# Performance work log

Measured on AMD Instinct MI355X. Metric: run time of the kernel, lower is better.

The kernel has to match this reference:

```python
import jax, jax.numpy as jnp
import numpy as np

N_NODES = 50000
N_EDGES = 800000
N_GRAPHS = 500
DIM = 64          # node feature dim
NG = 64           # num gaussians (edge rbf dim)
CUTOFF = 12.0
NCONV = 3
HID = 128
NTYPES = 100      # atom vocabulary for embedding
EPS = 1e-5        # batchnorm eps


def _bn(x, g, b):
    # training-mode batchnorm over the leading (edge/node) axis
    m = jnp.mean(x, axis=0)
    v = jnp.var(x, axis=0)
    return g * (x - m) * jax.lax.rsqrt(v + EPS) + b


def setup_inputs() -> dict:
    key = jax.random.key(0)
    ks = jax.random.split(key, 12)
    atom_types = jax.random.randint(ks[0], (N_NODES,), 0, NTYPES)
    src = jax.random.randint(ks[1], (N_EDGES,), 0, N_NODES)
    dst = jax.random.randint(ks[2], (N_EDGES,), 0, N_NODES)
    graph_ids = jnp.sort(jax.random.randint(ks[3], (N_NODES,), 0, N_GRAPHS))
    distance = jax.random.uniform(ks[4], (N_EDGES,), dtype=jnp.float32) * CUTOFF
    cin = 2 * DIM + NG
    s = 0.05
    embed_table = jax.random.normal(ks[5], (NTYPES, DIM), dtype=jnp.float32) * s
    W1 = jax.random.normal(ks[6], (NCONV, cin, DIM), dtype=jnp.float32) * s
    b1 = jnp.zeros((NCONV, DIM), jnp.float32)
    W2 = jax.random.normal(ks[7], (NCONV, cin, DIM), dtype=jnp.float32) * s
    b2 = jnp.zeros((NCONV, DIM), jnp.float32)
    g1 = jnp.ones((NCONV, DIM), jnp.float32); bt1 = jnp.zeros((NCONV, DIM), jnp.float32)
    g2 = jnp.ones((NCONV, DIM), jnp.float32); bt2 = jnp.zeros((NCONV, DIM), jnp.float32)
    g3 = jnp.ones((NCONV, DIM), jnp.float32); bt3 = jnp.zeros((NCONV, DIM), jnp.float32)
    Wfc = jax.random.normal(ks[8], (DIM, HID), dtype=jnp.float32) * s
    bfc = jnp.zeros((HID,), jnp.float32)
    Wout = jax.random.normal(ks[9], (HID, 1), dtype=jnp.float32) * s
    bout = jnp.zeros((1,), jnp.float32)
    return dict(atom_types=atom_types, src=src, dst=dst, graph_ids=graph_ids,
                distance=distance, embed_table=embed_table,
                W1=W1, b1=b1, W2=W2, b2=b2,
                g1=g1, bt1=bt1, g2=g2, bt2=bt2, g3=g3, bt3=bt3,
                Wfc=Wfc, bfc=bfc, Wout=Wout, bout=bout)


def reference(atom_types, src, dst, graph_ids, distance, embed_table,
              W1, b1, W2, b2, g1, bt1, g2, bt2, g3, bt3,
              Wfc, bfc, Wout, bout):
    # embedding lookup
    node = embed_table[atom_types]                           # [N, DIM]
    # RBF expansion of distances (gaussian smearing on [0, CUTOFF])
    mu = jnp.linspace(0.0, CUTOFF, NG, dtype=jnp.float32)
    coeff = -0.5 / (mu[1] - mu[0]) ** 2
    rbf = jnp.exp(coeff * (distance[:, None] - mu) ** 2)      # [E, NG]

    for i in range(NCONV):
        # gather: concat(src feats, dst feats, edge rbf)
        te = jnp.concatenate([node[src], node[dst], rbf], axis=-1)  # [E, 192]
        nbr_filter = jax.nn.sigmoid(_bn(te @ W1[i] + b1[i], g1[i], bt1[i]))
        # NOTE: faithful to the source bug: bn2 is applied to nbr_filter,
        # so fc_full2 (W2/b2) output is computed in torch but unused.
        nbr_core = jax.nn.softplus(_bn(nbr_filter, g2[i], bt2[i]))
        h = nbr_filter * nbr_core                              # [E, DIM]
        # scatter-sum messages to destination nodes
        agg = jax.ops.segment_sum(h, dst, num_segments=N_NODES)
        node = node + _bn(agg, g3[i], bt3[i])

    # avg pooling per graph
    sums = jax.ops.segment_sum(node, graph_ids, num_segments=N_GRAPHS)
    cnts = jax.ops.segment_sum(jnp.ones((N_NODES, 1), node.dtype), graph_ids,
                               num_segments=N_GRAPHS)
    crys = sums / jnp.maximum(cnts, 1.0)                       # [G, DIM]

    crys = jax.nn.softplus(crys) @ Wfc + bfc
    crys = jax.nn.softplus(crys)
    return crys @ Wout + bout                                  # [G, 1]
```

## Files before the change

### kernel.cpp

```cpp
#include <hip/hip_runtime.h>
#include <hip/hip_fp16.h>
#include <math.h>

#define DIM 64
#define NG 64
#define CIN 192
#define HID 128
#define NCONV 3
#define TB 2048
#define CUTOFF 12.0f
#define EPS 1e-5f
#define SCB 256

typedef int i2v __attribute__((ext_vector_type(2)));
typedef int i4v __attribute__((ext_vector_type(4)));

__device__ __forceinline__ float sp_(float y) {
    return fmaxf(y, 0.f) + __logf(1.f + __expf(-fabsf(y)));
}
__device__ __forceinline__ float sig_(float y) {
    return 1.f / (1.f + __expf(-y));
}
__device__ __forceinline__ float2 h2f2_bits(int bits) {
    __half2 h;
    __builtin_memcpy(&h, &bits, 4);
    return __half22float2(h);
}
__device__ __forceinline__ int f2h2_bits(float a, float b) {
    __half2 h;
    h.x = __float2half(a);
    h.y = __float2half(b);
    int r;
    __builtin_memcpy(&r, &h, 4);
    return r;
}

__global__ void k_tables(const float* __restrict__ W1, __half2* __restrict__ Tp) {
    int row = blockIdx.x;
    int l = row / TB, i = row % TB;
    int d = threadIdx.x;
    const float stepmu = CUTOFF / (float)(NG - 1);
    const float coeff = -0.5f / (stepmu * stepmu);
    const float stepx = CUTOFF / (float)(TB - 1);
    float x0 = (float)i * stepx;
    float x1 = fminf((float)(i + 1), (float)(TB - 1)) * stepx;
    __shared__ float r0[NG];
    __shared__ float r1[NG];
    float mu = (float)d * stepmu;
    float d0 = x0 - mu, d1 = x1 - mu;
    r0[d] = expf(coeff * d0 * d0);
    r1[d] = expf(coeff * d1 * d1);
    __syncthreads();
    const float* w = W1 + (size_t)(l * CIN + 2 * DIM) * DIM;
    float a0 = 0.f, a1 = 0.f;
#pragma unroll 8
    for (int g = 0; g < NG; ++g) {
        float wv = w[g * DIM + d];
        a0 += r0[g] * wv;
        a1 += r1[g] * wv;
    }
    __half2 hh;
    hh.x = __float2half(a0);
    hh.y = __float2half(a1);
    Tp[(size_t)row * DIM + d] = hh;
}

__global__ void k_hist(const int* __restrict__ dst, int* __restrict__ cnt, int E) {
    for (int e = blockIdx.x * blockDim.x + threadIdx.x; e < E;
         e += gridDim.x * blockDim.x)
        atomicAdd(&cnt[dst[e]], 1);
}

__global__ void k_scanA(const int* __restrict__ cnt, int* __restrict__ bsum, int N) {
    __shared__ int lds[SCB];
    int i = blockIdx.x * SCB + threadIdx.x;
    lds[threadIdx.x] = (i < N) ? cnt[i] : 0;
    __syncthreads();
    for (int o = SCB / 2; o > 0; o >>= 1) {
        if (threadIdx.x < o) lds[threadIdx.x] += lds[threadIdx.x + o];
        __syncthreads();
    }
    if (threadIdx.x == 0) bsum[blockIdx.x] = lds[0];
}

__global__ void k_scanB(const int* __restrict__ bsum, int* __restrict__ bexcl, int NB) {
    __shared__ int lds[SCB];
    int t = threadIdx.x;
    int v = (t < NB) ? bsum[t] : 0;
    lds[t] = v;
    __syncthreads();
    for (int o = 1; o < SCB; o <<= 1) {
        int add = (t >= o) ? lds[t - o] : 0;
        __syncthreads();
        lds[t] += add;
        __syncthreads();
    }
    if (t < NB) bexcl[t] = lds[t] - v;
}

__global__ void k_scanC(const int* __restrict__ cnt, const int* __restrict__ bexcl,
                        int* __restrict__ off, int* __restrict__ cursor, int N, int E) {
    __shared__ int lds[SCB];
    int t = threadIdx.x;
    int i = blockIdx.x * SCB + t;
    int v = (i < N) ? cnt[i] : 0;
    lds[t] = v;
    __syncthreads();
    for (int o = 1; o < SCB; o <<= 1) {
        int add = (t >= o) ? lds[t - o] : 0;
        __syncthreads();
        lds[t] += add;
        __syncthreads();
    }
    if (i < N) {
        int excl = bexcl[blockIdx.x] + lds[t] - v;
        off[i] = excl;
        cursor[i] = excl;
        if (i == N - 1) off[N] = E;
    }
}

__global__ void k_scatter(const int* __restrict__ src, const int* __restrict__ dst,
                          const float* __restrict__ dist, int* __restrict__ cursor,
                          int2* __restrict__ es, int E) {
    const float inv_step = (float)(TB - 1) / CUTOFF;
    for (int e = blockIdx.x * blockDim.x + threadIdx.x; e < E;
         e += gridDim.x * blockDim.x) {
        int t = dst[e];
        int pos = atomicAdd(&cursor[t], 1);
        es[pos] = make_int2(src[e], __float_as_int(dist[e] * inv_step));
    }
}

template <int FIRST>
__global__ void __launch_bounds__(256) k_pq(
        const int* __restrict__ at, const float* __restrict__ emb,
        float* __restrict__ node, const float* __restrict__ agg,
        const double* __restrict__ st, const float* __restrict__ g3,
        const float* __restrict__ bt3, double invN,
        const float* __restrict__ W1, const float* __restrict__ b1, int l,
        __half* __restrict__ P16, float* __restrict__ Q, int N) {
    __shared__ float wa[DIM * DIM];
    __shared__ float wb[DIM * DIM];
    const float* WA = W1 + (size_t)(l * CIN) * DIM;
    for (int k = threadIdx.x; k < DIM * DIM; k += blockDim.x) {
        wa[k] = WA[k];
        wb[k] = WA[DIM * DIM + k];
    }
    int lane = threadIdx.x & 63, w = threadIdx.x >> 6;
    float bv = b1[lane];
    float a3 = 0.f, c3 = 0.f;
    if (!FIRST) {
        double m = st[lane] * invN;
        double v = st[64 + lane] * invN - m * m;
        a3 = g3[lane] / sqrtf((float)v + EPS);
        c3 = bt3[lane] - a3 * (float)m;
    }
    __syncthreads();
    int wpb = blockDim.x >> 6;
    for (int n = blockIdx.x * wpb + w; n < N; n += gridDim.x * wpb) {
        float nv;
        if (FIRST) {
            nv = emb[at[n] * DIM + lane];
        } else {
            nv = node[n * DIM + lane] + a3 * agg[n * DIM + lane] + c3;
        }
        node[n * DIM + lane] = nv;
        float ap = 0.f, aq = bv;
#pragma unroll 8
        for (int k = 0; k < DIM; ++k) {
            float b = __shfl(nv, k);
            ap += b * wa[k * DIM + lane];
            aq += b * wb[k * DIM + lane];
        }
        P16[n * DIM + lane] = __float2half(ap);
        Q[n * DIM + lane] = aq;
    }
}

__global__ void __launch_bounds__(256) k_convA(
        const int* __restrict__ off, const int2* __restrict__ es,
        const __half* __restrict__ P16, const float* __restrict__ Q,
        const __half2* __restrict__ Tp,
        double* __restrict__ stats, __half* __restrict__ z16, int N) {
    int lane = threadIdx.x & 63;
    int w = threadIdx.x >> 6;
    int dg = lane & 15;
    int slot = lane >> 4;
    int d0 = dg * 4;
    float s00 = 0.f, s01 = 0.f, s02 = 0.f, s03 = 0.f;
    float s10 = 0.f, s11 = 0.f, s12 = 0.f, s13 = 0.f;
    int gw = blockIdx.x * 4 + w, nw = gridDim.x * 4;
    for (int n = gw; n < N; n += nw) {
        int e0 = off[n], e1 = off[n + 1];
        if (e0 >= e1) continue;
        float4 q4 = *(const float4*)(Q + (size_t)n * DIM + d0);
        for (int eb = e0; eb < e1; eb += 8) {
            int eA = eb + slot, eB = eA + 4;
            bool vA = (eA < e1), vB = (eB < e1);
            int2 evA = es[vA ? eA : e1 - 1];
            int2 evB = es[vB ? eB : e1 - 1];
            float uA = __int_as_float(evA.y), uB = __int_as_float(evB.y);
            int iA = (int)uA, iB = (int)uB;
            iA = max(0, min(iA, TB - 2));
            iB = max(0, min(iB, TB - 2));
            float frA = uA - (float)iA, frB = uB - (float)iB;
            i2v pbA = *(const i2v*)(P16 + (size_t)evA.x * DIM + d0);
            i2v pbB = *(const i2v*)(P16 + (size_t)evB.x * DIM + d0);
            i4v tbA = *(const i4v*)(Tp + (size_t)iA * DIM + d0);
            i4v tbB = *(const i4v*)(Tp + (size_t)iB * DIM + d0);
            {
                float2 p01 = h2f2_bits(pbA.x), p23 = h2f2_bits(pbA.y);
                float2 t0 = h2f2_bits(tbA.x), t1 = h2f2_bits(tbA.y);
                float2 t2 = h2f2_bits(tbA.z), t3 = h2f2_bits(tbA.w);
                float z0 = p01.x + t0.x + frA * (t0.y - t0.x) + q4.x;
                float z1 = p01.y + t1.x + frA * (t1.y - t1.x) + q4.y;
                float z2 = p23.x + t2.x + frA * (t2.y - t2.x) + q4.z;
                float z3 = p23.y + t3.x + frA * (t3.y - t3.x) + q4.w;
                if (vA) {
                    i2v zz;
                    zz.x = f2h2_bits(z0, z1);
                    zz.y = f2h2_bits(z2, z3);
                    *(i2v*)(z16 + (size_t)eA * DIM + d0) = zz;
                    s00 += z0; s10 += z0 * z0;
                    s01 += z1; s11 += z1 * z1;
                    s02 += z2; s12 += z2 * z2;
                    s03 += z3; s13 += z3 * z3;
                }
            }
            {
                float2 p01 = h2f2_bits(pbB.x), p23 = h2f2_bits(pbB.y);
                float2 t0 = h2f2_bits(tbB.x), t1 = h2f2_bits(tbB.y);
                float2 t2 = h2f2_bits(tbB.z), t3 = h2f2_bits(tbB.w);
                float z0 = p01.x + t0.x + frB * (t0.y - t0.x) + q4.x;
                float z1 = p01.y + t1.x + frB * (t1.y - t1.x) + q4.y;
                float z2 = p23.x + t2.x + frB * (t2.y - t2.x) + q4.z;
                float z3 = p23.y + t3.x + frB * (t3.y - t3.x) + q4.w;
                if (vB) {
                    i2v zz;
                    zz.x = f2h2_bits(z0, z1);
                    zz.y = f2h2_bits(z2, z3);
                    *(i2v*)(z16 + (size_t)eB * DIM + d0) = zz;
                    s00 += z0; s10 += z0 * z0;
                    s01 += z1; s11 += z1 * z1;
                    s02 += z2; s12 += z2 * z2;
                    s03 += z3; s13 += z3 * z3;
                }
            }
        }
    }
    __shared__ float r0[4][64][4];
    __shared__ float r1[4][64][4];
    r0[w][lane][0] = s00; r0[w][lane][1] = s01;
    r0[w][lane][2] = s02; r0[w][lane][3] = s03;
    r1[w][lane][0] = s10; r1[w][lane][1] = s11;
    r1[w][lane][2] = s12; r1[w][lane][3] = s13;
    __syncthreads();
    if (threadIdx.x < 64) {
        int d = threadIdx.x;
        int dgg = d >> 2, q = d & 3;
        float t0 = 0.f, t1 = 0.f;
#pragma unroll
        for (int ww = 0; ww < 4; ++ww)
#pragma unroll
            for (int sl = 0; sl < 4; ++sl) {
                t0 += r0[ww][sl * 16 + dgg][q];
                t1 += r1[ww][sl * 16 + dgg][q];
            }
        atomicAdd(&stats[d], (double)t0);
        atomicAdd(&stats[64 + d], (double)t1);
    }
}

__global__ void __launch_bounds__(256) k_statsF(
        __half* __restrict__ zf16,
        const double* __restrict__ stA, const float* __restrict__ gA,
        const float* __restrict__ btA,
        double* __restrict__ stats, int total8, double invE) {
    int gq = threadIdx.x & 7;
    float a1[8], c1[8];
#pragma unroll
    for (int q = 0; q < 8; ++q) {
        int d = gq * 8 + q;
        double m = stA[d] * invE;
        double v = stA[64 + d] * invE - m * m;
        a1[q] = gA[d] / sqrtf((float)v + EPS);
        c1[q] = btA[d] - a1[q] * (float)m;
    }
    float s0[8] = {0, 0, 0, 0, 0, 0, 0, 0};
    float s1[8] = {0, 0, 0, 0, 0, 0, 0, 0};
    i4v* z4 = (i4v*)zf16;
    int tid = blockIdx.x * blockDim.x + threadIdx.x;
    int stride = gridDim.x * blockDim.x;
    for (int i = tid; i < total8; i += stride) {
        i4v v = z4[i];
        float2 p0 = h2f2_bits(v.x);
        float2 p1 = h2f2_bits(v.y);
        float2 p2 = h2f2_bits(v.z);
        float2 p3 = h2f2_bits(v.w);
        float f0 = sig_(a1[0] * p0.x + c1[0]);
        float f1 = sig_(a1[1] * p0.y + c1[1]);
        float f2 = sig_(a1[2] * p1.x + c1[2]);
        float f3 = sig_(a1[3] * p1.y + c1[3]);
        float f4 = sig_(a1[4] * p2.x + c1[4]);
        float f5 = sig_(a1[5] * p2.y + c1[5]);
        float f6 = sig_(a1[6] * p3.x + c1[6]);
        float f7 = sig_(a1[7] * p3.y + c1[7]);
        i4v o;
        o.x = f2h2_bits(f0, f1);
        o.y = f2h2_bits(f2, f3);
        o.z = f2h2_bits(f4, f5);
        o.w = f2h2_bits(f6, f7);
        z4[i] = o;
        s0[0] += f0; s1[0] += f0 * f0;
        s0[1] += f1; s1[1] += f1 * f1;
        s0[2] += f2; s1[2] += f2 * f2;
        s0[3] += f3; s1[3] += f3 * f3;
        s0[4] += f4; s1[4] += f4 * f4;
        s0[5] += f5; s1[5] += f5 * f5;
        s0[6] += f6; s1[6] += f6 * f6;
        s0[7] += f7; s1[7] += f7 * f7;
    }
    __shared__ float lds[256][16];
#pragma unroll
    for (int q = 0; q < 8; ++q) {
        lds[threadIdx.x][q] = s0[q];
        lds[threadIdx.x][8 + q] = s1[q];
    }
    __syncthreads();
    if (threadIdx.x < 64) {
        int d = threadIdx.x;
        int grp = d >> 3, j = d & 7;
        float t0 = 0.f, t1 = 0.f;
        for (int k = 0; k < 32; ++k) {
            int t = k * 8 + grp;
            t0 += lds[t][j];
            t1 += lds[t][8 + j];
        }
        atomicAdd(&stats[d], (double)t0);
        atomicAdd(&stats[64 + d], (double)t1);
    }
}

__global__ void __launch_bounds__(256) k_aggF(
        const int* __restrict__ off, const __half* __restrict__ f16,
        const double* __restrict__ stB, const float* __restrict__ gB,
        const float* __restrict__ btB,
        double* __restrict__ stats, float* __restrict__ agg, int N, double invE) {
    int lane = threadIdx.x & 63;
    int w = threadIdx.x >> 6;
    int dg = lane & 7;
    int slot = lane >> 3;
    int d0 = dg * 8;
    float a2[8], c2[8];
#pragma unroll
    for (int q = 0; q < 8; ++q) {
        int d = d0 + q;
        double m = stB[d] * invE, v = stB[64 + d] * invE - m * m;
        a2[q] = gB[d] / sqrtf((float)v + EPS);
        c2[q] = btB[d] - a2[q] * (float)m;
    }
    float s0[8] = {0, 0, 0, 0, 0, 0, 0, 0};
    float s1[8] = {0, 0, 0, 0, 0, 0, 0, 0};
    int gw = blockIdx.x * 4 + w, nw = gridDim.x * 4;
    for (int n = gw; n < N; n += nw) {
        int e0 = off[n], e1 = off[n + 1];
        float tot[8] = {0, 0, 0, 0, 0, 0, 0, 0};
        for (int eb = e0; eb < e1; eb += 16) {
            int eA = eb + slot, eB = eA + 8;
            float mkA = (eA < e1) ? 1.f : 0.f;
            float mkB = (eB < e1) ? 1.f : 0.f;
            int ecA = (eA < e1) ? eA : (e1 - 1);
            int ecB = (eB < e1) ? eB : (e1 - 1);
            i4v zbA = *(const i4v*)(f16 + (size_t)ecA * DIM + d0);
            i4v zbB = *(const i4v*)(f16 + (size_t)ecB * DIM + d0);
            float2 a0 = h2f2_bits(zbA.x), a1v = h2f2_bits(zbA.y);
            float2 a2v = h2f2_bits(zbA.z), a3v = h2f2_bits(zbA.w);
            float2 b0 = h2f2_bits(zbB.x), b1v = h2f2_bits(zbB.y);
            float2 b2v = h2f2_bits(zbB.z), b3v = h2f2_bits(zbB.w);
            float fA[8] = {a0.x, a0.y, a1v.x, a1v.y, a2v.x, a2v.y, a3v.x, a3v.y};
            float fB[8] = {b0.x, b0.y, b1v.x, b1v.y, b2v.x, b2v.y, b3v.x, b3v.y};
#pragma unroll
            for (int q = 0; q < 8; ++q) {
                float hA = fA[q] * sp_(a2[q] * fA[q] + c2[q]);
                float hB = fB[q] * sp_(a2[q] * fB[q] + c2[q]);
                tot[q] += mkA * hA + mkB * hB;
            }
        }
#pragma unroll
        for (int q = 0; q < 8; ++q) {
            float v = tot[q];
            v += __shfl_xor(v, 8);
            v += __shfl_xor(v, 16);
            v += __shfl_xor(v, 32);
            tot[q] = v;
        }
        if (slot == 0) {
            float4 w0 = make_float4(tot[0], tot[1], tot[2], tot[3]);
            float4 w1 = make_float4(tot[4], tot[5], tot[6], tot[7]);
            *(float4*)(agg + (size_t)n * DIM + d0) = w0;
            *(float4*)(agg + (size_t)n * DIM + d0 + 4) = w1;
#pragma unroll
            for (int q = 0; q < 8; ++q) {
                s0[q] += tot[q];
                s1[q] += tot[q] * tot[q];
            }
        }
    }
    __shared__ float r0[4][8][8];
    __shared__ float r1[4][8][8];
    if (slot == 0) {
#pragma unroll
        for (int q = 0; q < 8; ++q) {
            r0[w][dg][q] = s0[q];
            r1[w][dg][q] = s1[q];
        }
    }
    __syncthreads();
    if (threadIdx.x < 64) {
        int d = threadIdx.x;
        int dgg = d >> 3, q = d & 7;
        float t0 = 0.f, t1 = 0.f;
#pragma unroll
        for (int ww = 0; ww < 4; ++ww) {
            t0 += r0[ww][dgg][q];
            t1 += r1[ww][dgg][q];
        }
        atomicAdd(&stats[d], (double)t0);
        atomicAdd(&stats[64 + d], (double)t1);
    }
}

template <int MODE>
__global__ void __launch_bounds__(256) k_conv(
        const int* __restrict__ off, const int2* __restrict__ es,
        const __half* __restrict__ P16, const float* __restrict__ Q,
        const __half2* __restrict__ Tp,
        const double* __restrict__ stA, const float* __restrict__ gA,
        const float* __restrict__ btA,
        const double* __restrict__ stB, const float* __restrict__ gB,
        const float* __restrict__ btB,
        double* __restrict__ stats, float* __restrict__ agg, int N, double invE) {
    int lane = threadIdx.x & 63;
    int w = threadIdx.x >> 6;
    float a1 = 0.f, c1 = 0.f, a2 = 0.f, c2 = 0.f;
    if (MODE >= 2) {
        double m = stA[lane] * invE;
        double v = stA[64 + lane] * invE - m * m;
        a1 = gA[lane] / sqrtf((float)v + EPS);
        c1 = btA[lane] - a1 * (float)m;
    }
    if (MODE == 3) {
        double m = stB[lane] * invE;
        double v = stB[64 + lane] * invE - m * m;
        a2 = gB[lane] / sqrtf((float)v + EPS);
        c2 = btB[lane] - a2 * (float)m;
    }
    float s0 = 0.f, s1 = 0.f;
    int gw = blockIdx.x * 4 + w, nw = gridDim.x * 4;
    for (int n = gw; n < N; n += nw) {
        int e0 = off[n], e1 = off[n + 1];
        float qc = Q[n * DIM + lane];
        float acc = 0.f;
        auto body = [&](int2 ev) {
            float u = __int_as_float(ev.y);
            int i = (int)u;
            i = max(0, min(i, TB - 2));
            float fr = u - (float)i;
            float2 t2 = __half22float2(Tp[(size_t)i * DIM + lane]);
            float p = __half2float(P16[(size_t)ev.x * DIM + lane]);
            float z = p + t2.x + fr * (t2.y - t2.x) + qc;
            if (MODE == 0) { s0 += z; s1 += z * z; }
            else {
                float f = sig_(a1 * z + c1);
                if (MODE == 2) { s0 += f; s1 += f * f; }
                else acc += f * sp_(a2 * f + c2);
            }
        };
        int e = e0;
        for (; e + 2 <= e1; e += 2) { body(es[e]); body(es[e + 1]); }
        if (e < e1) body(es[e]);
        if (MODE == 3) {
            agg[n * DIM + lane] = acc;
            s0 += acc; s1 += acc * acc;
        }
    }
    __shared__ float r0[4][64];
    __shared__ float r1[4][64];
    r0[w][lane] = s0;
    r1[w][lane] = s1;
    __syncthreads();
    if (threadIdx.x < 64) {
        int d = threadIdx.x;
        float t0 = r0[0][d] + r0[1][d] + r0[2][d] + r0[3][d];
        float t1 = r1[0][d] + r1[1][d] + r1[2][d] + r1[3][d];
        atomicAdd(&stats[d], (double)t0);
        atomicAdd(&stats[64 + d], (double)t1);
    }
}

__global__ void k_head(const float* __restrict__ node, const float* __restrict__ agg,
                       const double* __restrict__ st, const float* __restrict__ g3,
                       const float* __restrict__ bt3, double invN,
                       const int* __restrict__ gid, int N,
                       const float* __restrict__ Wfc, const float* __restrict__ bfc,
                       const float* __restrict__ Wout, const float* __restrict__ bout,
                       float* __restrict__ out) {
    int g = blockIdx.x;
    __shared__ int bounds[2];
    if (threadIdx.x == 0) {
        int lo = 0, hi = N;
        while (lo < hi) { int mid = (lo + hi) >> 1; if (gid[mid] < g) lo = mid + 1; else hi = mid; }
        bounds[0] = lo;
        int lo2 = lo; hi = N;
        while (lo2 < hi) { int mid = (lo2 + hi) >> 1; if (gid[mid] < g + 1) lo2 = mid + 1; else hi = mid; }
        bounds[1] = lo2;
    }
    __syncthreads();
    int s = bounds[0], e = bounds[1];
    __shared__ float sp[DIM];
    if (threadIdx.x < DIM) {
        int d = threadIdx.x;
        double mm = st[d] * invN;
        double vv = st[64 + d] * invN - mm * mm;
        float a3 = g3[d] / sqrtf((float)vv + EPS);
        float c3 = bt3[d] - a3 * (float)mm;
        float sn = 0.f, sa = 0.f;
        for (int n = s; n < e; ++n) {
            sn += node[(size_t)n * DIM + d];
            sa += agg[(size_t)n * DIM + d];
        }
        float cntf = (float)max(e - s, 1);
        float m = (sn + a3 * sa) / cntf + c3;
        sp[d] = (m > 0.f) ? m + log1pf(expf(-m)) : log1pf(expf(m));
    }
    __syncthreads();
    int j = threadIdx.x;
    float hj = bfc[j];
#pragma unroll 8
    for (int k = 0; k < DIM; ++k) hj += sp[k] * Wfc[k * HID + j];
    hj = (hj > 0.f) ? hj + log1pf(expf(-hj)) : log1pf(expf(hj));
    __shared__ float red[HID];
    red[j] = hj * Wout[j];
    __syncthreads();
    for (int o = HID / 2; o > 0; o >>= 1) {
        if (j < o) red[j] += red[j + o];
        __syncthreads();
    }
    if (j == 0) out[g] = red[0] + bout[0];
}

extern "C" void kernel_launch(void* const* d_in, const int* in_sizes, int n_in,
                              void* d_out, int out_size, void* d_ws, size_t ws_size,
                              hipStream_t stream) {
    const int* atom_types = (const int*)d_in[0];
    const int* src = (const int*)d_in[1];
    const int* dst = (const int*)d_in[2];
    const int* gid = (const int*)d_in[3];
    const float* dist = (const float*)d_in[4];
    const float* emb = (const float*)d_in[5];
    const float* W1 = (const float*)d_in[6];
    const float* b1 = (const float*)d_in[7];
    const float* g1 = (const float*)d_in[10];
    const float* bt1 = (const float*)d_in[11];
    const float* g2 = (const float*)d_in[12];
    const float* bt2 = (const float*)d_in[13];
    const float* g3 = (const float*)d_in[14];
    const float* bt3 = (const float*)d_in[15];
    const float* Wfc = (const float*)d_in[16];
    const float* bfc = (const float*)d_in[17];
    const float* Wout = (const float*)d_in[18];
    const float* bout = (const float*)d_in[19];

    int N = in_sizes[0];
    int E = in_sizes[1];
    int G = out_size;
    int NB = (N + SCB - 1) / SCB;

    char* ws = (char*)d_ws;
    auto alloc = [&](size_t bytes) -> char* {
        char* p = ws;
        ws += (bytes + 255) & ~(size_t)255;
        return p;
    };
    size_t nd = (size_t)N * DIM * sizeof(float);
    float* node = (float*)alloc(nd);
    __half* P16 = (__half*)alloc(nd / 2);
    float* Q = (float*)alloc(nd);
    float* agg = (float*)alloc(nd);
    __half2* Tp = (__half2*)alloc((size_t)NCONV * TB * DIM * sizeof(__half2));
    double* stats = (double*)alloc((size_t)NCONV * 3 * 128 * sizeof(double));
    int* off = (int*)alloc((size_t)(N + 1) * sizeof(int));
    int* cursor = (int*)alloc((size_t)N * sizeof(int));
    int* cnt = (int*)alloc((size_t)N * sizeof(int));
    int* bsum = (int*)alloc(SCB * sizeof(int));
    int* bexcl = (int*)alloc(SCB * sizeof(int));
    int2* es = (int2*)alloc((size_t)E * sizeof(int2));
    size_t zbytes = (size_t)E * DIM * sizeof(__half);
    size_t used = (size_t)(ws - (char*)d_ws);
    bool planZ = (used + zbytes) <= ws_size;
    __half* z16 = planZ ? (__half*)alloc(zbytes) : nullptr;

    hipMemsetAsync(stats, 0, (size_t)NCONV * 3 * 128 * sizeof(double), stream);
    hipMemsetAsync(cnt, 0, (size_t)N * sizeof(int), stream);

    k_tables<<<NCONV * TB, 64, 0, stream>>>(W1, Tp);

    k_hist<<<1024, 256, 0, stream>>>(dst, cnt, E);
    k_scanA<<<NB, SCB, 0, stream>>>(cnt, bsum, N);
    k_scanB<<<1, SCB, 0, stream>>>(bsum, bexcl, NB);
    k_scanC<<<NB, SCB, 0, stream>>>(cnt, bexcl, off, cursor, N, E);
    k_scatter<<<1024, 256, 0, stream>>>(src, dst, dist, cursor, es, E);

    double invE = 1.0 / (double)E;
    double invN = 1.0 / (double)N;

    for (int l = 0; l < NCONV; ++l) {
        const __half2* Tl = Tp + (size_t)l * TB * DIM;
        double* st1 = stats + (size_t)(l * 3 + 0) * 128;
        double* st2 = stats + (size_t)(l * 3 + 1) * 128;
        double* st3 = stats + (size_t)(l * 3 + 2) * 128;

        if (l == 0) {
            k_pq<1><<<2048, 256, 0, stream>>>(atom_types, emb, node, nullptr,
                                              nullptr, nullptr, nullptr, 0.0,
                                              W1, b1 + l * DIM, l, P16, Q, N);
        } else {
            double* st3p = stats + (size_t)((l - 1) * 3 + 2) * 128;
            k_pq<0><<<2048, 256, 0, stream>>>(atom_types, emb, node, agg,
                                              st3p, g3 + (l - 1) * DIM,
                                              bt3 + (l - 1) * DIM, invN,
                                              W1, b1 + l * DIM, l, P16, Q, N);
        }

        if (planZ) {
            k_convA<<<2048, 256, 0, stream>>>(off, es, P16, Q, Tl, st1, z16, N);
            k_statsF<<<2048, 256, 0, stream>>>(z16, st1, g1 + l * DIM, bt1 + l * DIM,
                                               st2, E * 8, invE);
            k_aggF<<<2048, 256, 0, stream>>>(off, z16,
                                             st2, g2 + l * DIM, bt2 + l * DIM,
                                             st3, agg, N, invE);
        } else {
            k_conv<0><<<2048, 256, 0, stream>>>(off, es, P16, Q, Tl,
                                                nullptr, nullptr, nullptr,
                                                nullptr, nullptr, nullptr,
                                                st1, nullptr, N, invE);
            k_conv<2><<<2048, 256, 0, stream>>>(off, es, P16, Q, Tl,
                                                st1, g1 + l * DIM, bt1 + l * DIM,
                                                nullptr, nullptr, nullptr,
                                                st2, nullptr, N, invE);
            k_conv<3><<<2048, 256, 0, stream>>>(off, es, P16, Q, Tl,
                                                st1, g1 + l * DIM, bt1 + l * DIM,
                                                st2, g2 + l * DIM, bt2 + l * DIM,
                                                st3, agg, N, invE);
        }
    }

    double* st3f = stats + (size_t)(2 * 3 + 2) * 128;
    k_head<<<G, HID, 0, stream>>>(node, agg, st3f, g3 + 2 * DIM, bt3 + 2 * DIM,
                                  invN, gid, N, Wfc, bfc, Wout, bout, (float*)d_out);
}
```

Measured before the change: 971.8 us.

## Flatten edge conv pass over edges and merge scan into one kernel

The first conv pass now loops over the CSR-sorted edges in flat chunks of 8 instead of one wavefront per destination node. It reads each edge's destination from a new dst_s array written during the scatter step, which removes load imbalance from uneven node degrees and the tail waste on low-degree nodes. The cost is an extra per-edge index read plus one Q gather per edge instead of one per node. The three-kernel scan is also replaced by a single 1024-thread block scan, which cuts two launches but runs serially per thread over about 49 elements.

```diff
diff --git a/kernel.cpp b/kernel.cpp
--- a/kernel.cpp
+++ b/kernel.cpp
@@ -10,7 +10,6 @@
 #define TB 2048
 #define CUTOFF 12.0f
 #define EPS 1e-5f
-#define SCB 256
 
 typedef int i2v __attribute__((ext_vector_type(2)));
 typedef int i4v __attribute__((ext_vector_type(4)));
@@ -71,64 +70,43 @@
         atomicAdd(&cnt[dst[e]], 1);
 }
 
-__global__ void k_scanA(const int* __restrict__ cnt, int* __restrict__ bsum, int N) {
-    __shared__ int lds[SCB];
-    int i = blockIdx.x * SCB + threadIdx.x;
-    lds[threadIdx.x] = (i < N) ? cnt[i] : 0;
-    __syncthreads();
-    for (int o = SCB / 2; o > 0; o >>= 1) {
-        if (threadIdx.x < o) lds[threadIdx.x] += lds[threadIdx.x + o];
+__global__ void __launch_bounds__(1024) k_scan(const int* __restrict__ cnt,
+                                               int* __restrict__ off,
+                                               int* __restrict__ cursor,
+                                               int N, int E) {
+    __shared__ int psum[1024];
+    int t = threadIdx.x;
+    int C = (N + 1023) / 1024;
+    int lo = t * C, hi = min(lo + C, N);
+    int s = 0;
+    for (int i = lo; i < hi; ++i) s += cnt[i];
+    psum[t] = s;
+    __syncthreads();
+    for (int o = 1; o < 1024; o <<= 1) {
+        int add = (t >= o) ? psum[t - o] : 0;
         __syncthreads();
-    }
-    if (threadIdx.x == 0) bsum[blockIdx.x] = lds[0];
-}
-
-__global__ void k_scanB(const int* __restrict__ bsum, int* __restrict__ bexcl, int NB) {
-    __shared__ int lds[SCB];
-    int t = threadIdx.x;
-    int v = (t < NB) ? bsum[t] : 0;
-    lds[t] = v;
-    __syncthreads();
-    for (int o = 1; o < SCB; o <<= 1) {
-        int add = (t >= o) ? lds[t - o] : 0;
+        psum[t] += add;
         __syncthreads();
-        lds[t] += add;
-        __syncthreads();
-    }
-    if (t < NB) bexcl[t] = lds[t] - v;
-}
-
-__global__ void k_scanC(const int* __restrict__ cnt, const int* __restrict__ bexcl,
-                        int* __restrict__ off, int* __restrict__ cursor, int N, int E) {
-    __shared__ int lds[SCB];
-    int t = threadIdx.x;
-    int i = blockIdx.x * SCB + t;
-    int v = (i < N) ? cnt[i] : 0;
-    lds[t] = v;
-    __syncthreads();
-    for (int o = 1; o < SCB; o <<= 1) {
-        int add = (t >= o) ? lds[t - o] : 0;
-        __syncthreads();
-        lds[t] += add;
-        __syncthreads();
-    }
-    if (i < N) {
-        int excl = bexcl[blockIdx.x] + lds[t] - v;
-        off[i] = excl;
-        cursor[i] = excl;
-        if (i == N - 1) off[N] = E;
-    }
+    }
+    int run = psum[t] - s;
+    for (int i = lo; i < hi; ++i) {
+        off[i] = run;
+        cursor[i] = run;
+        run += cnt[i];
+    }
+    if (t == 1023) off[N] = E;
 }
 
 __global__ void k_scatter(const int* __restrict__ src, const int* __restrict__ dst,
                           const float* __restrict__ dist, int* __restrict__ cursor,
-                          int2* __restrict__ es, int E) {
+                          int2* __restrict__ es, int* __restrict__ dst_s, int E) {
     const float inv_step = (float)(TB - 1) / CUTOFF;
     for (int e = blockIdx.x * blockDim.x + threadIdx.x; e < E;
          e += gridDim.x * blockDim.x) {
         int t = dst[e];
         int pos = atomicAdd(&cursor[t], 1);
         es[pos] = make_int2(src[e], __float_as_int(dist[e] * inv_step));
+        dst_s[pos] = t;
     }
 }
 
@@ -160,11 +138,8 @@
     int wpb = blockDim.x >> 6;
     for (int n = blockIdx.x * wpb + w; n < N; n += gridDim.x * wpb) {
         float nv;
-        if (FIRST) {
-            nv = emb[at[n] * DIM + lane];
-        } else {
-            nv = node[n * DIM + lane] + a3 * agg[n * DIM + lane] + c3;
-        }
+        if (FIRST) nv = emb[at[n] * DIM + lane];
+        else nv = node[n * DIM + lane] + a3 * agg[n * DIM + lane] + c3;
         node[n * DIM + lane] = nv;
         float ap = 0.f, aq = bv;
 #pragma unroll 8
@@ -178,74 +153,73 @@
     }
 }
 
-__global__ void __launch_bounds__(256) k_convA(
-        const int* __restrict__ off, const int2* __restrict__ es,
+__global__ void __launch_bounds__(256) k_convAf(
+        const int2* __restrict__ es, const int* __restrict__ dst_s,
         const __half* __restrict__ P16, const float* __restrict__ Q,
         const __half2* __restrict__ Tp,
-        double* __restrict__ stats, __half* __restrict__ z16, int N) {
+        double* __restrict__ stats, __half* __restrict__ z16, int E) {
     int lane = threadIdx.x & 63;
     int w = threadIdx.x >> 6;
-    int dg = lane & 15;
-    int slot = lane >> 4;
+    int dg = lane & 15, slot = lane >> 4;
     int d0 = dg * 4;
     float s00 = 0.f, s01 = 0.f, s02 = 0.f, s03 = 0.f;
     float s10 = 0.f, s11 = 0.f, s12 = 0.f, s13 = 0.f;
     int gw = blockIdx.x * 4 + w, nw = gridDim.x * 4;
-    for (int n = gw; n < N; n += nw) {
-        int e0 = off[n], e1 = off[n + 1];
-        if (e0 >= e1) continue;
-        float4 q4 = *(const float4*)(Q + (size_t)n * DIM + d0);
-        for (int eb = e0; eb < e1; eb += 8) {
-            int eA = eb + slot, eB = eA + 4;
-            bool vA = (eA < e1), vB = (eB < e1);
-            int2 evA = es[vA ? eA : e1 - 1];
-            int2 evB = es[vB ? eB : e1 - 1];
-            float uA = __int_as_float(evA.y), uB = __int_as_float(evB.y);
-            int iA = (int)uA, iB = (int)uB;
-            iA = max(0, min(iA, TB - 2));
-            iB = max(0, min(iB, TB - 2));
-            float frA = uA - (float)iA, frB = uB - (float)iB;
-            i2v pbA = *(const i2v*)(P16 + (size_t)evA.x * DIM + d0);
-            i2v pbB = *(const i2v*)(P16 + (size_t)evB.x * DIM + d0);
-            i4v tbA = *(const i4v*)(Tp + (size_t)iA * DIM + d0);
-            i4v tbB = *(const i4v*)(Tp + (size_t)iB * DIM + d0);
-            {
-                float2 p01 = h2f2_bits(pbA.x), p23 = h2f2_bits(pbA.y);
-                float2 t0 = h2f2_bits(tbA.x), t1 = h2f2_bits(tbA.y);
-                float2 t2 = h2f2_bits(tbA.z), t3 = h2f2_bits(tbA.w);
-                float z0 = p01.x + t0.x + frA * (t0.y - t0.x) + q4.x;
-                float z1 = p01.y + t1.x + frA * (t1.y - t1.x) + q4.y;
-                float z2 = p23.x + t2.x + frA * (t2.y - t2.x) + q4.z;
-                float z3 = p23.y + t3.x + frA * (t3.y - t3.x) + q4.w;
-                if (vA) {
-                    i2v zz;
-                    zz.x = f2h2_bits(z0, z1);
-                    zz.y = f2h2_bits(z2, z3);
-                    *(i2v*)(z16 + (size_t)eA * DIM + d0) = zz;
-                    s00 += z0; s10 += z0 * z0;
-                    s01 += z1; s11 += z1 * z1;
-                    s02 += z2; s12 += z2 * z2;
-                    s03 += z3; s13 += z3 * z3;
-                }
+    for (int eb = gw * 8; eb < E; eb += nw * 8) {
+        int eA = eb + slot, eB = eA + 4;
+        bool vA = (eA < E), vB = (eB < E);
+        int ecA = vA ? eA : E - 1;
+        int ecB = vB ? eB : E - 1;
+        int2 evA = es[ecA];
+        int2 evB = es[ecB];
+        int dA = dst_s[ecA], dB = dst_s[ecB];
+        float uA = __int_as_float(evA.y), uB = __int_as_float(evB.y);
+        int iA = (int)uA, iB = (int)uB;
+        iA = max(0, min(iA, TB - 2));
+        iB = max(0, min(iB, TB - 2));
+        float frA = uA - (float)iA, frB = uB - (float)iB;
+        i2v pbA = *(const i2v*)(P16 + (size_t)evA.x * DIM + d0);
+        i2v pbB = *(const i2v*)(P16 + (size_t)evB.x * DIM + d0);
+        i4v tbA = *(const i4v*)(Tp + (size_t)iA * DIM + d0);
+        i4v tbB = *(const i4v*)(Tp + (size_t)iB * DIM + d0);
+        float4 qA = *(const float4*)(Q + (size_t)dA * DIM + d0);
+        float4 qB = *(const float4*)(Q + (size_t)dB * DIM + d0);
+        {
+            float2 p01 = h2f2_bits(pbA.x), p23 = h2f2_bits(pbA.y);
+            float2 t0 = h2f2_bits(tbA.x), t1 = h2f2_bits(tbA.y);
+            float2 t2 = h2f2_bits(tbA.z), t3 = h2f2_bits(tbA.w);
+            float z0 = p01.x + t0.x + frA * (t0.y - t0.x) + qA.x;
+            float z1 = p01.y + t1.x + frA * (t1.y - t1.x) + qA.y;
+            float z2 = p23.x + t2.x + frA * (t2.y - t2.x) + qA.z;
+            float z3 = p23.y + t3.x + frA * (t3.y - t3.x) + qA.w;
+            if (vA) {
+                i2v zz;
+                zz.x = f2h2_bits(z0, z1);
+                zz.y = f2h2_bits(z2, z3);
+                *(i2v*)(z16 + (size_t)eA * DIM + d0) = zz;
+                s00 += z0; s10 += z0 * z0;
+                s01 += z1; s11 += z1 * z1;
+                s02 += z2; s12 += z2 * z2;
+                s03 += z3; s13 += z3 * z3;
             }
-            {
-                float2 p01 = h2f2_bits(pbB.x), p23 = h2f2_bits(pbB.y);
-                float2 t0 = h2f2_bits(tbB.x), t1 = h2f2_bits(tbB.y);
-                float2 t2 = h2f2_bits(tbB.z), t3 = h2f2_bits(tbB.w);
-                float z0 = p01.x + t0.x + frB * (t0.y - t0.x) + q4.x;
-                float z1 = p01.y + t1.x + frB * (t1.y - t1.x) + q4.y;
-                float z2 = p23.x + t2.x + frB * (t2.y - t2.x) + q4.z;
-                float z3 = p23.y + t3.x + frB * (t3.y - t3.x) + q4.w;
-                if (vB) {
-                    i2v zz;
-                    zz.x = f2h2_bits(z0, z1);
-                    zz.y = f2h2_bits(z2, z3);
-                    *(i2v*)(z16 + (size_t)eB * DIM + d0) = zz;
-                    s00 += z0; s10 += z0 * z0;
-                    s01 += z1; s11 += z1 * z1;
-                    s02 += z2; s12 += z2 * z2;
-                    s03 += z3; s13 += z3 * z3;
-                }
+        }
+        {
+            float2 p01 = h2f2_bits(pbB.x), p23 = h2f2_bits(pbB.y);
+            float2 t0 = h2f2_bits(tbB.x), t1 = h2f2_bits(tbB.y);
+            float2 t2 = h2f2_bits(tbB.z), t3 = h2f2_bits(tbB.w);
+            float z0 = p01.x + t0.x + frB * (t0.y - t0.x) + qB.x;
+            float z1 = p01.y + t1.x + frB * (t1.y - t1.x) + qB.y;
+            float z2 = p23.x + t2.x + frB * (t2.y - t2.x) + qB.z;
+            float z3 = p23.y + t3.x + frB * (t3.y - t3.x) + qB.w;
+            if (vB) {
+                i2v zz;
+                zz.x = f2h2_bits(z0, z1);
+                zz.y = f2h2_bits(z2, z3);
+                *(i2v*)(z16 + (size_t)eB * DIM + d0) = zz;
+                s00 += z0; s10 += z0 * z0;
+                s01 += z1; s11 += z1 * z1;
+                s02 += z2; s12 += z2 * z2;
+                s03 += z3; s13 += z3 * z3;
             }
         }
     }
@@ -349,8 +323,7 @@
         double* __restrict__ stats, float* __restrict__ agg, int N, double invE) {
     int lane = threadIdx.x & 63;
     int w = threadIdx.x >> 6;
-    int dg = lane & 7;
-    int slot = lane >> 3;
+    int dg = lane & 7, slot = lane >> 3;
     int d0 = dg * 8;
     float a2[8], c2[8];
 #pragma unroll
@@ -429,6 +402,57 @@
         atomicAdd(&stats[d], (double)t0);
         atomicAdd(&stats[64 + d], (double)t1);
     }
+}
+
+__global__ void k_head(const float* __restrict__ node, const float* __restrict__ agg,
+                       const double* __restrict__ st, const float* __restrict__ g3,
+                       const float* __restrict__ bt3, double invN,
+                       const int* __restrict__ gid, int N,
+                       const float* __restrict__ Wfc, const float* __restrict__ bfc,
+                       const float* __restrict__ Wout, const float* __restrict__ bout,
+                       float* __restrict__ out) {
+    int g = blockIdx.x;
+    __shared__ int bounds[2];
+    if (threadIdx.x == 0) {
+        int lo = 0, hi = N;
+        while (lo < hi) { int mid = (lo + hi) >> 1; if (gid[mid] < g) lo = mid + 1; else hi = mid; }
+        bounds[0] = lo;
+        int lo2 = lo; hi = N;
+        while (lo2 < hi) { int mid = (lo2 + hi) >> 1; if (gid[mid] < g + 1) lo2 = mid + 1; else hi = mid; }
+        bounds[1] = lo2;
+    }
+    __syncthreads();
+    int s = bounds[0], e = bounds[1];
+    __shared__ float sp[DIM];
+    if (threadIdx.x < DIM) {
+        int d = threadIdx.x;
+        double mm = st[d] * invN;
+        double vv = st[64 + d] * invN - mm * mm;
+        float a3 = g3[d] / sqrtf((float)vv + EPS);
+        float c3 = bt3[d] - a3 * (float)mm;
+        float sn = 0.f, sa = 0.f;
+        for (int n = s; n < e; ++n) {
+            sn += node[(size_t)n * DIM + d];
+            sa += agg[(size_t)n * DIM + d];
+        }
+        float cntf = (float)max(e - s, 1);
+        float m = (sn + a3 * sa) / cntf + c3;
+        sp[d] = (m > 0.f) ? m + log1pf(expf(-m)) : log1pf(expf(m));
+    }
+    __syncthreads();
+    int j = threadIdx.x;
+    float hj = bfc[j];
+#pragma unroll 8
+    for (int k = 0; k < DIM; ++k) hj += sp[k] * Wfc[k * HID + j];
+    hj = (hj > 0.f) ? hj + log1pf(expf(-hj)) : log1pf(expf(hj));
+    __shared__ float red[HID];
+    red[j] = hj * Wout[j];
+    __syncthreads();
+    for (int o = HID / 2; o > 0; o >>= 1) {
+        if (j < o) red[j] += red[j + o];
+        __syncthreads();
+    }
+    if (j == 0) out[g] = red[0] + bout[0];
 }
 
 template <int MODE>
@@ -499,57 +523,6 @@
     }
 }
 
-__global__ void k_head(const float* __restrict__ node, const float* __restrict__ agg,
-                       const double* __restrict__ st, const float* __restrict__ g3,
-                       const float* __restrict__ bt3, double invN,
-                       const int* __restrict__ gid, int N,
-                       const float* __restrict__ Wfc, const float* __restrict__ bfc,
-                       const float* __restrict__ Wout, const float* __restrict__ bout,
-                       float* __restrict__ out) {
-    int g = blockIdx.x;
-    __shared__ int bounds[2];
-    if (threadIdx.x == 0) {
-        int lo = 0, hi = N;
-        while (lo < hi) { int mid = (lo + hi) >> 1; if (gid[mid] < g) lo = mid + 1; else hi = mid; }
-        bounds[0] = lo;
-        int lo2 = lo; hi = N;
-        while (lo2 < hi) { int mid = (lo2 + hi) >> 1; if (gid[mid] < g + 1) lo2 = mid + 1; else hi = mid; }
-        bounds[1] = lo2;
-    }
-    __syncthreads();
-    int s = bounds[0], e = bounds[1];
-    __shared__ float sp[DIM];
-    if (threadIdx.x < DIM) {
-        int d = threadIdx.x;
-        double mm = st[d] * invN;
-        double vv = st[64 + d] * invN - mm * mm;
-        float a3 = g3[d] / sqrtf((float)vv + EPS);
-        float c3 = bt3[d] - a3 * (float)mm;
-        float sn = 0.f, sa = 0.f;
-        for (int n = s; n < e; ++n) {
-            sn += node[(size_t)n * DIM + d];
-            sa += agg[(size_t)n * DIM + d];
-        }
-        float cntf = (float)max(e - s, 1);
-        float m = (sn + a3 * sa) / cntf + c3;
-        sp[d] = (m > 0.f) ? m + log1pf(expf(-m)) : log1pf(expf(m));
-    }
-    __syncthreads();
-    int j = threadIdx.x;
-    float hj = bfc[j];
-#pragma unroll 8
-    for (int k = 0; k < DIM; ++k) hj += sp[k] * Wfc[k * HID + j];
-    hj = (hj > 0.f) ? hj + log1pf(expf(-hj)) : log1pf(expf(hj));
-    __shared__ float red[HID];
-    red[j] = hj * Wout[j];
-    __syncthreads();
-    for (int o = HID / 2; o > 0; o >>= 1) {
-        if (j < o) red[j] += red[j + o];
-        __syncthreads();
-    }
-    if (j == 0) out[g] = red[0] + bout[0];
-}
-
 extern "C" void kernel_launch(void* const* d_in, const int* in_sizes, int n_in,
                               void* d_out, int out_size, void* d_ws, size_t ws_size,
                               hipStream_t stream) {
@@ -575,7 +548,6 @@
     int N = in_sizes[0];
     int E = in_sizes[1];
     int G = out_size;
-    int NB = (N + SCB - 1) / SCB;
 
     char* ws = (char*)d_ws;
     auto alloc = [&](size_t bytes) -> char* {
@@ -593,9 +565,8 @@
     int* off = (int*)alloc((size_t)(N + 1) * sizeof(int));
     int* cursor = (int*)alloc((size_t)N * sizeof(int));
     int* cnt = (int*)alloc((size_t)N * sizeof(int));
-    int* bsum = (int*)alloc(SCB * sizeof(int));
-    int* bexcl = (int*)alloc(SCB * sizeof(int));
     int2* es = (int2*)alloc((size_t)E * sizeof(int2));
+    int* dst_s = (int*)alloc((size_t)E * sizeof(int));
     size_t zbytes = (size_t)E * DIM * sizeof(__half);
     size_t used = (size_t)(ws - (char*)d_ws);
     bool planZ = (used + zbytes) <= ws_size;
@@ -605,12 +576,9 @@
     hipMemsetAsync(cnt, 0, (size_t)N * sizeof(int), stream);
 
     k_tables<<<NCONV * TB, 64, 0, stream>>>(W1, Tp);
-
     k_hist<<<1024, 256, 0, stream>>>(dst, cnt, E);
-    k_scanA<<<NB, SCB, 0, stream>>>(cnt, bsum, N);
-    k_scanB<<<1, SCB, 0, stream>>>(bsum, bexcl, NB);
-    k_scanC<<<NB, SCB, 0, stream>>>(cnt, bexcl, off, cursor, N, E);
-    k_scatter<<<1024, 256, 0, stream>>>(src, dst, dist, cursor, es, E);
+    k_scan<<<1, 1024, 0, stream>>>(cnt, off, cursor, N, E);
+    k_scatter<<<1024, 256, 0, stream>>>(src, dst, dist, cursor, es, dst_s, E);
 
     double invE = 1.0 / (double)E;
     double invN = 1.0 / (double)N;
@@ -634,7 +602,7 @@
         }
 
         if (planZ) {
-            k_convA<<<2048, 256, 0, stream>>>(off, es, P16, Q, Tl, st1, z16, N);
+            k_convAf<<<2048, 256, 0, stream>>>(es, dst_s, P16, Q, Tl, st1, z16, E);
             k_statsF<<<2048, 256, 0, stream>>>(z16, st1, g1 + l * DIM, bt1 + l * DIM,
                                                st2, E * 8, invE);
             k_aggF<<<2048, 256, 0, stream>>>(off, z16,
```

After: 1.062 ms. 9.3% more time.
